# Kernel tuning notes

Hardware: AMD Instinct MI355X
Metric: run time of the kernel (lower is better)

## Reference

```python
import jax, jax.numpy as jnp
import numpy as np

H = 512   # hidden_size
V = 5000  # output_size (vocab)
B = 128   # batch
S = 64    # encoder source length
T = 52    # max_trajectory_length


def setup_inputs() -> dict:
    key = jax.random.key(0)
    ks = jax.random.split(key, 16)
    sc = 0.05
    rn = lambda k, shape: jax.random.normal(k, shape, dtype=jnp.float32) * sc
    return dict(
        encoder_outputs=jax.random.normal(ks[0], (B, S, H), dtype=jnp.float32),
        h0=jax.random.normal(ks[1], (1, B, H), dtype=jnp.float32),
        c0=jax.random.normal(ks[2], (1, B, H), dtype=jnp.float32),
        target_tensor=jax.random.randint(ks[3], (B, T), 0, V),
        emb=rn(ks[4], (V, H)),
        Wa=rn(ks[5], (H, H)), ba=jnp.zeros((H,), jnp.float32),
        Ua=rn(ks[6], (H, H)), bu=jnp.zeros((H,), jnp.float32),
        Va=rn(ks[7], (H,)), bv=jnp.zeros((), jnp.float32),
        W_ih=rn(ks[8], (4 * H, 2 * H)), W_hh=rn(ks[9], (4 * H, H)),
        b_ih=jnp.zeros((4 * H,), jnp.float32), b_hh=jnp.zeros((4 * H,), jnp.float32),
        Wout=rn(ks[10], (V, H)), bout=jnp.zeros((V,), jnp.float32),
    )


def reference(encoder_outputs, h0, c0, target_tensor, emb,
              Wa, ba, Ua, bu, Va, bv,
              W_ih, W_hh, b_ih, b_hh, Wout, bout):
    # Dropout is identity in eval mode.
    b = target_tensor.shape[0]
    # Ua(keys) is constant across decode steps -> precompute once. [B,S,H]
    keys_proj = jnp.einsum('bsh,kh->bsk', encoder_outputs, Ua) + bu
    # Teacher forcing: input at step i is target[:, i-1], step 0 is token 0.
    tokens = jnp.concatenate(
        [jnp.zeros((b, 1), target_tensor.dtype), target_tensor[:, :-1]], axis=1)  # [B,T]

    def step(carry, tok):
        h, c = carry                                # [B,H] each
        x = emb[tok]                                # embedding lookup [B,H]
        q = h @ Wa.T + ba                           # Wa(query) [B,H]
        scores = jnp.tanh(q[:, None, :] + keys_proj) @ Va + bv  # [B,S]
        w = jax.nn.softmax(scores, axis=-1)         # attn weights [B,S]
        ctx = jnp.einsum('bs,bsh->bh', w, encoder_outputs)       # context [B,H]
        xi = jnp.concatenate([x, ctx], axis=-1)     # [B,2H]
        gates = xi @ W_ih.T + b_ih + h @ W_hh.T + b_hh           # [B,4H]
        i_g, f_g, g_g, o_g = jnp.split(gates, 4, axis=-1)        # torch gate order i,f,g,o
        c = jax.nn.sigmoid(f_g) * c + jax.nn.sigmoid(i_g) * jnp.tanh(g_g)
        h = jax.nn.sigmoid(o_g) * jnp.tanh(c)
        logits = h @ Wout.T + bout                  # [B,V]
        return (h, c), (logits, w)

    (h, c), (logits, attn) = jax.lax.scan(step, (h0[0], c0[0]), tokens.T)
    logits = jnp.transpose(logits, (1, 0, 2))       # [B,T,V]
    log_probs = jax.nn.log_softmax(logits, axis=-1)
    attn = jnp.transpose(attn, (1, 0, 2))           # [B,T,S]
    return log_probs, (h[None], c[None]), attn
```

## Files before the change

kernel.cpp:

```cpp
#include <hip/hip_runtime.h>
#include <math.h>

#define H 512
#define V 5000
#define BB 128
#define SS 64
#define TT 52
#define NB 160

typedef __attribute__((ext_vector_type(8))) short bf16x8;
typedef __attribute__((ext_vector_type(4))) float f32x4;
typedef __attribute__((ext_vector_type(2))) float f32x2;

__device__ __forceinline__ unsigned short f2b(float f) {
    unsigned u = __float_as_uint(f);
    return (unsigned short)((u + 0x7fffu + ((u >> 16) & 1u)) >> 16);
}
__device__ __forceinline__ float b2f(unsigned short u) {
    return __uint_as_float((unsigned)u << 16);
}
__device__ __forceinline__ float ftanh(float x) {
    return 1.f - 2.f / (1.f + __expf(2.f * x));
}
__device__ __forceinline__ float fsig(float x) {
    return 1.f / (1.f + __expf(-x));
}
__device__ __forceinline__ unsigned char f2fp8(float f) {
    return (unsigned char)__builtin_amdgcn_cvt_pk_fp8_f32(f, f, 0, 0);
}

__device__ __forceinline__ void cld_row16(const unsigned short* p, bf16x8* r)
{
    asm volatile(
        "global_load_dwordx4 %0, %16, off sc0 sc1\n\t"
        "global_load_dwordx4 %1, %16, off offset:64 sc0 sc1\n\t"
        "global_load_dwordx4 %2, %16, off offset:128 sc0 sc1\n\t"
        "global_load_dwordx4 %3, %16, off offset:192 sc0 sc1\n\t"
        "global_load_dwordx4 %4, %16, off offset:256 sc0 sc1\n\t"
        "global_load_dwordx4 %5, %16, off offset:320 sc0 sc1\n\t"
        "global_load_dwordx4 %6, %16, off offset:384 sc0 sc1\n\t"
        "global_load_dwordx4 %7, %16, off offset:448 sc0 sc1\n\t"
        "global_load_dwordx4 %8, %16, off offset:512 sc0 sc1\n\t"
        "global_load_dwordx4 %9, %16, off offset:576 sc0 sc1\n\t"
        "global_load_dwordx4 %10, %16, off offset:640 sc0 sc1\n\t"
        "global_load_dwordx4 %11, %16, off offset:704 sc0 sc1\n\t"
        "global_load_dwordx4 %12, %16, off offset:768 sc0 sc1\n\t"
        "global_load_dwordx4 %13, %16, off offset:832 sc0 sc1\n\t"
        "global_load_dwordx4 %14, %16, off offset:896 sc0 sc1\n\t"
        "global_load_dwordx4 %15, %16, off offset:960 sc0 sc1\n\t"
        "s_waitcnt vmcnt(0)"
        : "=v"(r[0]), "=v"(r[1]), "=v"(r[2]), "=v"(r[3]),
          "=v"(r[4]), "=v"(r[5]), "=v"(r[6]), "=v"(r[7]),
          "=v"(r[8]), "=v"(r[9]), "=v"(r[10]), "=v"(r[11]),
          "=v"(r[12]), "=v"(r[13]), "=v"(r[14]), "=v"(r[15])
        : "v"(p) : "memory");
}
__device__ __forceinline__ void cld_f_2(const float* p0, const float* p1,
                                        float& a, float& b)
{
    asm volatile(
        "global_load_dword %0, %2, off sc0 sc1\n\t"
        "global_load_dword %1, %3, off sc0 sc1\n\t"
        "s_waitcnt vmcnt(0)"
        : "=v"(a), "=v"(b) : "v"(p0), "v"(p1) : "memory");
}
__device__ __forceinline__ void cld_f4p(const float* p, f32x4& a, f32x4& b)
{
    asm volatile(
        "global_load_dwordx4 %0, %2, off sc0 sc1\n\t"
        "global_load_dwordx4 %1, %2, off offset:16 sc0 sc1\n\t"
        "s_waitcnt vmcnt(0)"
        : "=v"(a), "=v"(b) : "v"(p) : "memory");
}
__device__ __forceinline__ void cst_f(float* p, float v)
{
    asm volatile("global_store_dword %0, %1, off sc0 sc1"
                 :: "v"(p), "v"(v) : "memory");
}
__device__ __forceinline__ void cst_u32(unsigned* p, unsigned v)
{
    asm volatile("global_store_dword %0, %1, off sc0 sc1"
                 :: "v"(p), "v"(v) : "memory");
}
__device__ __forceinline__ void cst_h(unsigned short* p, unsigned short v)
{
    unsigned vv = v;
    asm volatile("global_store_short %0, %1, off sc0 sc1"
                 :: "v"(p), "v"(vv) : "memory");
}

__global__ __launch_bounds__(256)
void prep_w(const float* __restrict__ Wa, const float* __restrict__ Whh,
            const float* __restrict__ Wih,
            const float* __restrict__ ba, const float* __restrict__ bih,
            const float* __restrict__ bhh,
            const float* __restrict__ Ua, const float* __restrict__ Wout,
            const float* __restrict__ enc,
            unsigned short* __restrict__ Wbig, unsigned short* __restrict__ Wc,
            unsigned short* __restrict__ Uab, unsigned short* __restrict__ Woutb,
            unsigned short* __restrict__ encb, float* __restrict__ bbig)
{
    const int stride = gridDim.x * blockDim.x;
    const int t0 = blockIdx.x * blockDim.x + threadIdx.x;
    for (int idx = t0; idx < 2560 * 1024; idx += stride) {
        const int j = idx >> 10, k = idx & 1023;
        float v;
        if (j < H) v = (k < H) ? Wa[j * H + k] : 0.f;
        else { const int n = j - H; v = (k < H) ? Whh[n * H + k] : Wih[n * 2 * H + (k - H)]; }
        Wbig[idx] = f2b(v);
    }
    for (int idx = t0; idx < 2048 * 512; idx += stride) {
        const int n = idx >> 9, k = idx & 511;
        Wc[idx] = f2b(Wih[n * 2 * H + H + k]);
    }
    for (int idx = t0; idx < 512 * 512; idx += stride)   Uab[idx]   = f2b(Ua[idx]);
    for (int idx = t0; idx < V * 512; idx += stride)     Woutb[idx] = f2b(Wout[idx]);
    for (int idx = t0; idx < BB * SS * H; idx += stride) encb[idx]  = f2b(enc[idx]);
    for (int j = t0; j < 2560; j += stride)
        bbig[j] = (j < H) ? ba[j] : bih[j - H] + bhh[j - H];
}

__global__ __launch_bounds__(256)
void gather_x(const float* __restrict__ emb, const int* __restrict__ tgt,
              unsigned short* __restrict__ xall)
{
    const int stride = gridDim.x * blockDim.x;
    for (int idx = blockIdx.x * blockDim.x + threadIdx.x; idx < TT * BB * H; idx += stride) {
        const int k = idx & 511;
        const int row = idx >> 9;
        const int t = row >> 7, b = row & 127;
        const int tok = (t == 0) ? 0 : tgt[b * TT + t - 1];
        xall[idx] = f2b(emb[(size_t)tok * H + k]);
    }
}

template<int OUT_MODE, int PERMUTE>
__global__ __launch_bounds__(256, 2)
void gemm_mfma(const unsigned short* __restrict__ A,
               const unsigned short* __restrict__ B,
               const float* __restrict__ bias,
               float* __restrict__ Cf, unsigned short* __restrict__ Cb,
               unsigned char* __restrict__ C8,
               int M, int N)
{
    __shared__ unsigned short As[128][72];
    __shared__ unsigned short Bs[128][72];
    const int tid = threadIdx.x;
    const int m0 = blockIdx.y * 128, n0 = blockIdx.x * 128;
    const int lane = tid & 63, wv = tid >> 6;
    const int qm = (wv >> 1) * 64, qn = (wv & 1) * 64;
    const int fr = lane & 15, fg = lane >> 4;
    f32x4 acc[4][4];
#pragma unroll
    for (int i = 0; i < 4; ++i)
#pragma unroll
        for (int j = 0; j < 4; ++j) acc[i][j] = (f32x4){0.f, 0.f, 0.f, 0.f};

    const int srow = tid >> 3, sc = (tid & 7) * 8;
    for (int k0 = 0; k0 < H; k0 += 64) {
#pragma unroll
        for (int u = 0; u < 4; ++u) {
            const int row = srow + u * 32;
            *(uint4*)&As[row][sc] = *(const uint4*)&A[(size_t)(m0 + row) * H + k0 + sc];
            int nr = n0 + row; if (nr > N - 1) nr = N - 1;
            *(uint4*)&Bs[row][sc] = *(const uint4*)&B[(size_t)nr * H + k0 + sc];
        }
        __syncthreads();
#pragma unroll
        for (int ks = 0; ks < 2; ++ks) {
            const int kk = ks * 32 + fg * 8;
            bf16x8 av[4], bv[4];
#pragma unroll
            for (int i = 0; i < 4; ++i) {
                av[i] = *(const bf16x8*)&As[qm + i * 16 + fr][kk];
                bv[i] = *(const bf16x8*)&Bs[qn + i * 16 + fr][kk];
            }
#pragma unroll
            for (int i = 0; i < 4; ++i)
#pragma unroll
                for (int j = 0; j < 4; ++j)
                    acc[i][j] = __builtin_amdgcn_mfma_f32_16x16x32_bf16(av[i], bv[j], acc[i][j], 0, 0, 0);
        }
        __syncthreads();
    }
#pragma unroll
    for (int i = 0; i < 4; ++i) {
        const int r0 = m0 + qm + i * 16 + fg * 4;
#pragma unroll
        for (int j = 0; j < 4; ++j) {
            const int col = n0 + qn + j * 16 + fr;
            if (col < N) {
                const float bi = bias ? bias[col] : 0.f;
#pragma unroll
                for (int v = 0; v < 4; ++v) {
                    const int r = r0 + v;
                    const float val = acc[i][j][v] + bi;
                    if (OUT_MODE == 1) {
                        Cb[(size_t)r * N + col] = f2b(val);
                    } else if (OUT_MODE == 2) {
                        C8[(size_t)r * N + col] = f2fp8(val);
                    } else {
                        const size_t orow = PERMUTE ? ((size_t)(r & (BB - 1)) * TT + (r >> 7))
                                                    : (size_t)r;
                        Cf[orow * (size_t)N + col] = val;
                    }
                }
            }
        }
    }
}

__device__ __forceinline__ void signal_flag(unsigned* flags, unsigned step)
{
    __syncthreads();
    if (threadIdx.x == 0)
        __hip_atomic_store(&flags[blockIdx.x * 32], step, __ATOMIC_RELAXED,
                           __HIP_MEMORY_SCOPE_AGENT);
}
__device__ __forceinline__ void wait_flags(unsigned* flags, int lo, int hi,
                                           unsigned step)
{
    for (int i = lo + (int)threadIdx.x; i < hi; i += 256) {
        while (__hip_atomic_load(&flags[i * 32], __ATOMIC_RELAXED,
                                 __HIP_MEMORY_SCOPE_AGENT) < step)
            __builtin_amdgcn_s_sleep(1);
    }
    __syncthreads();
}

struct PParams {
    const float* h0;
    const float* c0;
    const unsigned short* keysb;
    const unsigned char* encW8;
    const float* Va;
    const float* bv;
    const float* bbig;
    const unsigned short* Wbig;
    const unsigned short* xall;
    unsigned short* hbf;
    float* Y;
    unsigned short* hallb;
    float* attn;
    float* out_h;
    float* out_c;
    unsigned* flags;
};

__global__ __launch_bounds__(256, 1)
void persist(PParams p)
{
    __shared__ unsigned short WA[16][1032];
    __shared__ float qa_s[H];
    __shared__ float va_s[H];
    __shared__ float part[SS][4];
    __shared__ float wbuf[SS];
    __shared__ float gbuf[4 * H];
    __shared__ float cs[H];

    const int tid  = threadIdx.x;
    const int beta = blockIdx.x;
    unsigned bs = 1;

    for (int i = beta * 256 + tid; i < BB * H; i += NB * 256)
        cst_h(&p.hbf[i], f2b(p.h0[i]));
    {
        const int j0 = beta * 16;
        for (int idx = tid; idx < 16 * 128; idx += 256) {
            const int r = idx >> 7, ch = idx & 127;
            *(uint4*)&WA[r][ch * 8] = *(const uint4*)&p.Wbig[(size_t)(j0 + r) * 1024 + ch * 8];
        }
    }
    if (beta < 128) {
        for (int j = tid; j < H; j += 256) cs[j] = p.c0[beta * H + j];
        for (int i = tid; i < H; i += 256) va_s[i] = p.Va[i];
    }
    signal_flag(p.flags, bs);
    wait_flags(p.flags, 0, NB, bs);
    ++bs;

    for (int t = 0; t < TT; ++t) {
        {
            const int j0 = beta * 16;
            const int wv = tid >> 6, lane = tid & 63;
            const int r = lane & 15, g = lane >> 4;
            const int b0 = wv * 32, b1 = b0 + 16;
            const int ko = g * 8;
            bf16x8 hr0[16], hr1[16];
            cld_row16(p.hbf + (size_t)(b0 + r) * H + ko, hr0);
            cld_row16(p.hbf + (size_t)(b1 + r) * H + ko, hr1);
            f32x4 acc0 = {0.f, 0.f, 0.f, 0.f};
            f32x4 acc1 = {0.f, 0.f, 0.f, 0.f};
#pragma unroll
            for (int ks = 0; ks < 16; ++ks) {
                bf16x8 bf = *(const bf16x8*)&WA[r][ks * 32 + ko];
                acc0 = __builtin_amdgcn_mfma_f32_16x16x32_bf16(hr0[ks], bf, acc0, 0, 0, 0);
                acc1 = __builtin_amdgcn_mfma_f32_16x16x32_bf16(hr1[ks], bf, acc1, 0, 0, 0);
            }
            const unsigned short* x0p = p.xall + ((size_t)t * BB + b0 + r) * H + ko;
            const unsigned short* x1p = p.xall + ((size_t)t * BB + b1 + r) * H + ko;
#pragma unroll
            for (int ks = 0; ks < 16; ++ks) {
                bf16x8 bf = *(const bf16x8*)&WA[r][512 + ks * 32 + ko];
                acc0 = __builtin_amdgcn_mfma_f32_16x16x32_bf16(*(const bf16x8*)&x0p[ks * 32], bf, acc0, 0, 0, 0);
                acc1 = __builtin_amdgcn_mfma_f32_16x16x32_bf16(*(const bf16x8*)&x1p[ks * 32], bf, acc1, 0, 0, 0);
            }
            const float bb = p.bbig[j0 + r];
#pragma unroll
            for (int i = 0; i < 4; ++i) {
                cst_f(p.Y + (size_t)(b0 + g * 4 + i) * 2560 + j0 + r, acc0[i] + bb);
                cst_f(p.Y + (size_t)(b1 + g * 4 + i) * 2560 + j0 + r, acc1[i] + bb);
            }
        }
        signal_flag(p.flags, bs);

        if (beta < 128) {
            const int b = beta;
            const float* yrow = p.Y + (size_t)b * 2560;
            wait_flags(p.flags, 0, 32, bs);
            cld_f_2(yrow + tid, yrow + 256 + tid, qa_s[tid], qa_s[tid + 256]);
            __syncthreads();
            const int s = tid >> 2, q = tid & 3;
            const unsigned short* kp = p.keysb + ((size_t)b * SS + s) * H + q * 128;
            const float* qp = qa_s + q * 128;
            const float* vp = va_s + q * 128;
            float a2 = 0.f, a2b = 0.f;
#pragma unroll 4
            for (int i = 0; i < 128; i += 2) {
                a2  += ftanh(qp[i] + b2f(kp[i])) * vp[i];
                a2b += ftanh(qp[i + 1] + b2f(kp[i + 1])) * vp[i + 1];
            }
            part[s][q] = a2 + a2b;
            __syncthreads();
            if (tid < 64) {
                float sc = part[tid][0] + part[tid][1] + part[tid][2] + part[tid][3] + p.bv[0];
                float m = sc;
                for (int o = 32; o; o >>= 1) m = fmaxf(m, __shfl_xor(m, o));
                const float e = __expf(sc - m);
                float ss = e;
                for (int o = 32; o; o >>= 1) ss += __shfl_xor(ss, o);
                const float w = e / ss;
                wbuf[tid] = w;
                p.attn[((size_t)b * TT + t) * SS + tid] = w;
            }
            wait_flags(p.flags, 32, NB, bs);
            {
                float gc[8] = {0.f, 0.f, 0.f, 0.f, 0.f, 0.f, 0.f, 0.f};
                const unsigned char* ew = p.encW8 + (size_t)b * SS * 2048 + tid * 8;
#pragma unroll 8
                for (int s2 = 0; s2 < SS; ++s2) {
                    const float w2 = wbuf[s2];
                    const uint2 u = *(const uint2*)(ew + (size_t)s2 * 2048);
                    const f32x2 e01 = __builtin_amdgcn_cvt_pk_f32_fp8(u.x, 0);
                    const f32x2 e23 = __builtin_amdgcn_cvt_pk_f32_fp8(u.x, 1);
                    const f32x2 e45 = __builtin_amdgcn_cvt_pk_f32_fp8(u.y, 0);
                    const f32x2 e67 = __builtin_amdgcn_cvt_pk_f32_fp8(u.y, 1);
                    gc[0] += w2 * e01[0]; gc[1] += w2 * e01[1];
                    gc[2] += w2 * e23[0]; gc[3] += w2 * e23[1];
                    gc[4] += w2 * e45[0]; gc[5] += w2 * e45[1];
                    gc[6] += w2 * e67[0]; gc[7] += w2 * e67[1];
                }
                f32x4 y0, y1;
                cld_f4p(yrow + 512 + tid * 8, y0, y1);
#pragma unroll
                for (int i = 0; i < 4; ++i) {
                    gbuf[tid * 8 + i]     = gc[i] + y0[i];
                    gbuf[tid * 8 + 4 + i] = gc[4 + i] + y1[i];
                }
            }
            __syncthreads();
            {
                const int last = (t == TT - 1);
                unsigned hpack = 0;
                float hn2[2], cn2[2];
#pragma unroll
                for (int u = 0; u < 2; ++u) {
                    const int j = tid * 2 + u;
                    const float ig = gbuf[j];
                    const float fg = gbuf[512 + j];
                    const float gg = gbuf[1024 + j];
                    const float og = gbuf[1536 + j];
                    const float co = cs[j];
                    const float cn = fsig(fg) * co + fsig(ig) * ftanh(gg);
                    const float hn = fsig(og) * ftanh(cn);
                    cs[j] = cn;
                    hn2[u] = hn; cn2[u] = cn;
                    hpack |= ((unsigned)f2b(hn)) << (16 * u);
                }
                cst_u32((unsigned*)&p.hbf[b * H + tid * 2], hpack);
                *(unsigned*)&p.hallb[((size_t)t * BB + b) * H + tid * 2] = hpack;
                if (last) {
#pragma unroll
                    for (int u = 0; u < 2; ++u) {
                        p.out_h[b * H + tid * 2 + u] = hn2[u];
                        p.out_c[b * H + tid * 2 + u] = cn2[u];
                    }
                }
            }
        }
        signal_flag(p.flags, bs + 1);
        wait_flags(p.flags, 0, NB, bs + 1);
        bs += 2;
    }
}

__global__ __launch_bounds__(256)
void logsoftmax_rows(float* __restrict__ P)
{
    __shared__ float red[256];
    float* p = P + (size_t)blockIdx.x * V;
    const int tid = threadIdx.x;
    float m = -1e30f;
    for (int i = tid; i < V; i += 256) m = fmaxf(m, p[i]);
    red[tid] = m; __syncthreads();
    for (int sft = 128; sft; sft >>= 1) {
        if (tid < sft) red[tid] = fmaxf(red[tid], red[tid + sft]);
        __syncthreads();
    }
    m = red[0]; __syncthreads();
    float ssum = 0.f;
    for (int i = tid; i < V; i += 256) ssum += __expf(p[i] - m);
    red[tid] = ssum; __syncthreads();
    for (int sft = 128; sft; sft >>= 1) {
        if (tid < sft) red[tid] += red[tid + sft];
        __syncthreads();
    }
    const float lse = m + __logf(red[0]);
    for (int i = tid; i < V; i += 256) p[i] -= lse;
}

extern "C" void kernel_launch(void* const* d_in, const int* in_sizes, int n_in,
                              void* d_out, int out_size, void* d_ws, size_t ws_size,
                              hipStream_t stream)
{
    (void)in_sizes; (void)n_in; (void)out_size; (void)ws_size;
    const float* enc  = (const float*)d_in[0];
    const float* h0   = (const float*)d_in[1];
    const float* c0   = (const float*)d_in[2];
    const int*   tgt  = (const int*)  d_in[3];
    const float* emb  = (const float*)d_in[4];
    const float* Wa   = (const float*)d_in[5];
    const float* ba   = (const float*)d_in[6];
    const float* Ua   = (const float*)d_in[7];
    const float* bu   = (const float*)d_in[8];
    const float* Va   = (const float*)d_in[9];
    const float* bv   = (const float*)d_in[10];
    const float* Wih  = (const float*)d_in[11];
    const float* Whh  = (const float*)d_in[12];
    const float* bih  = (const float*)d_in[13];
    const float* bhh  = (const float*)d_in[14];
    const float* Wout = (const float*)d_in[15];
    const float* bout = (const float*)d_in[16];

    float* ws = (float*)d_ws;
    float* Y    = ws;
    float* bbig = Y + 327680;
    unsigned* flags = (unsigned*)(bbig + 2560);
    unsigned short* Wbig  = (unsigned short*)(flags + 5504);
    unsigned short* Wc    = Wbig + 2621440;
    unsigned short* Uab   = Wc + 1048576;
    unsigned short* Woutb = Uab + 262144;
    unsigned short* encb  = Woutb + 2560000;
    unsigned short* keysb = encb + 4194304;
    unsigned short* xall  = keysb + 4194304;
    unsigned short* hallb = xall + 3407872;
    unsigned short* hbf   = hallb + 3407872;
    unsigned char*  encW8 = (unsigned char*)(hbf + 65536);

    float* out    = (float*)d_out;
    float* out_h  = out + (size_t)BB * TT * V;
    float* out_c  = out_h + BB * H;
    float* out_at = out_c + BB * H;

    hipMemsetAsync(flags, 0, 5504 * sizeof(unsigned), stream);

    prep_w<<<dim3(2048), dim3(256), 0, stream>>>(
        Wa, Whh, Wih, ba, bih, bhh, Ua, Wout, enc, Wbig, Wc, Uab, Woutb, encb, bbig);
    gather_x<<<dim3(512), dim3(256), 0, stream>>>(emb, tgt, xall);

    gemm_mfma<1, 0><<<dim3(4, 64), dim3(256), 0, stream>>>(
        encb, Uab, bu, nullptr, keysb, nullptr, BB * SS, H);
    gemm_mfma<2, 0><<<dim3(16, 64), dim3(256), 0, stream>>>(
        encb, Wc, nullptr, nullptr, nullptr, encW8, BB * SS, 2048);

    PParams pp;
    pp.h0 = h0; pp.c0 = c0; pp.keysb = keysb; pp.encW8 = encW8;
    pp.Va = Va; pp.bv = bv; pp.bbig = bbig;
    pp.Wbig = Wbig; pp.xall = xall;
    pp.hbf = hbf; pp.Y = Y; pp.hallb = hallb;
    pp.attn = out_at; pp.out_h = out_h; pp.out_c = out_c;
    pp.flags = flags;
    persist<<<dim3(NB), dim3(256), 0, stream>>>(pp);

    gemm_mfma<0, 1><<<dim3(40, 52), dim3(256), 0, stream>>>(
        hallb, Woutb, bout, out, nullptr, nullptr, TT * BB, V);
    logsoftmax_rows<<<dim3(BB * TT), dim3(256), 0, stream>>>(out);
}
```

Baseline: 1.465 ms.

## Replace per-step global barrier with fine-grained per-row flag waits

Drops the end-of-step all-block barrier. Each wave now waits only on the flags of the 32 batch rows whose hidden state it reads before loading them. Block-to-column assignment is remapped so the last 32 blocks compute the query projection, and the attention blocks wait only on those before starting. The two row loads are issued back-to-back with a single wait, and the flag protocol gains a separate per-step hidden-ready signal. This trades the global barrier's latency for more complex dependency tracking, with the risk of ordering or visibility bugs.

```diff
diff --git a/kernel.cpp b/kernel.cpp
--- a/kernel.cpp
+++ b/kernel.cpp
@@ -29,31 +29,37 @@
     return (unsigned char)__builtin_amdgcn_cvt_pk_fp8_f32(f, f, 0, 0);
 }
 
+#define CLD16_BODY \
+        "global_load_dwordx4 %0, %16, off sc0 sc1\n\t"              \
+        "global_load_dwordx4 %1, %16, off offset:64 sc0 sc1\n\t"    \
+        "global_load_dwordx4 %2, %16, off offset:128 sc0 sc1\n\t"   \
+        "global_load_dwordx4 %3, %16, off offset:192 sc0 sc1\n\t"   \
+        "global_load_dwordx4 %4, %16, off offset:256 sc0 sc1\n\t"   \
+        "global_load_dwordx4 %5, %16, off offset:320 sc0 sc1\n\t"   \
+        "global_load_dwordx4 %6, %16, off offset:384 sc0 sc1\n\t"   \
+        "global_load_dwordx4 %7, %16, off offset:448 sc0 sc1\n\t"   \
+        "global_load_dwordx4 %8, %16, off offset:512 sc0 sc1\n\t"   \
+        "global_load_dwordx4 %9, %16, off offset:576 sc0 sc1\n\t"   \
+        "global_load_dwordx4 %10, %16, off offset:640 sc0 sc1\n\t"  \
+        "global_load_dwordx4 %11, %16, off offset:704 sc0 sc1\n\t"  \
+        "global_load_dwordx4 %12, %16, off offset:768 sc0 sc1\n\t"  \
+        "global_load_dwordx4 %13, %16, off offset:832 sc0 sc1\n\t"  \
+        "global_load_dwordx4 %14, %16, off offset:896 sc0 sc1\n\t"  \
+        "global_load_dwordx4 %15, %16, off offset:960 sc0 sc1"
+#define CLD16_OUTS(r) \
+          "=v"(r[0]), "=v"(r[1]), "=v"(r[2]), "=v"(r[3]),   \
+          "=v"(r[4]), "=v"(r[5]), "=v"(r[6]), "=v"(r[7]),   \
+          "=v"(r[8]), "=v"(r[9]), "=v"(r[10]), "=v"(r[11]), \
+          "=v"(r[12]), "=v"(r[13]), "=v"(r[14]), "=v"(r[15])
+
+__device__ __forceinline__ void cld_row16_nw(const unsigned short* p, bf16x8* r)
+{
+    asm volatile(CLD16_BODY : CLD16_OUTS(r) : "v"(p) : "memory");
+}
 __device__ __forceinline__ void cld_row16(const unsigned short* p, bf16x8* r)
 {
-    asm volatile(
-        "global_load_dwordx4 %0, %16, off sc0 sc1\n\t"
-        "global_load_dwordx4 %1, %16, off offset:64 sc0 sc1\n\t"
-        "global_load_dwordx4 %2, %16, off offset:128 sc0 sc1\n\t"
-        "global_load_dwordx4 %3, %16, off offset:192 sc0 sc1\n\t"
-        "global_load_dwordx4 %4, %16, off offset:256 sc0 sc1\n\t"
-        "global_load_dwordx4 %5, %16, off offset:320 sc0 sc1\n\t"
-        "global_load_dwordx4 %6, %16, off offset:384 sc0 sc1\n\t"
-        "global_load_dwordx4 %7, %16, off offset:448 sc0 sc1\n\t"
-        "global_load_dwordx4 %8, %16, off offset:512 sc0 sc1\n\t"
-        "global_load_dwordx4 %9, %16, off offset:576 sc0 sc1\n\t"
-        "global_load_dwordx4 %10, %16, off offset:640 sc0 sc1\n\t"
-        "global_load_dwordx4 %11, %16, off offset:704 sc0 sc1\n\t"
-        "global_load_dwordx4 %12, %16, off offset:768 sc0 sc1\n\t"
-        "global_load_dwordx4 %13, %16, off offset:832 sc0 sc1\n\t"
-        "global_load_dwordx4 %14, %16, off offset:896 sc0 sc1\n\t"
-        "global_load_dwordx4 %15, %16, off offset:960 sc0 sc1\n\t"
-        "s_waitcnt vmcnt(0)"
-        : "=v"(r[0]), "=v"(r[1]), "=v"(r[2]), "=v"(r[3]),
-          "=v"(r[4]), "=v"(r[5]), "=v"(r[6]), "=v"(r[7]),
-          "=v"(r[8]), "=v"(r[9]), "=v"(r[10]), "=v"(r[11]),
-          "=v"(r[12]), "=v"(r[13]), "=v"(r[14]), "=v"(r[15])
-        : "v"(p) : "memory");
+    asm volatile(CLD16_BODY "\n\ts_waitcnt vmcnt(0)"
+                 : CLD16_OUTS(r) : "v"(p) : "memory");
 }
 __device__ __forceinline__ void cld_f_2(const float* p0, const float* p1,
                                         float& a, float& b)
@@ -226,6 +232,16 @@
             __builtin_amdgcn_s_sleep(1);
     }
     __syncthreads();
+}
+__device__ __forceinline__ void wait_flags_wave32(unsigned* flags, int lo,
+                                                  unsigned step)
+{
+    const int lane = threadIdx.x & 63;
+    if (lane < 32) {
+        while (__hip_atomic_load(&flags[(lo + lane) * 32], __ATOMIC_RELAXED,
+                                 __HIP_MEMORY_SCOPE_AGENT) < step)
+            __builtin_amdgcn_s_sleep(1);
+    }
 }
 
 struct PParams {
@@ -260,35 +276,34 @@
 
     const int tid  = threadIdx.x;
     const int beta = blockIdx.x;
-    unsigned bs = 1;
+    const int j0   = (beta < 128) ? (512 + beta * 16) : ((beta - 128) * 16);
 
     for (int i = beta * 256 + tid; i < BB * H; i += NB * 256)
         cst_h(&p.hbf[i], f2b(p.h0[i]));
-    {
-        const int j0 = beta * 16;
-        for (int idx = tid; idx < 16 * 128; idx += 256) {
-            const int r = idx >> 7, ch = idx & 127;
-            *(uint4*)&WA[r][ch * 8] = *(const uint4*)&p.Wbig[(size_t)(j0 + r) * 1024 + ch * 8];
-        }
+    for (int idx = tid; idx < 16 * 128; idx += 256) {
+        const int r = idx >> 7, ch = idx & 127;
+        *(uint4*)&WA[r][ch * 8] = *(const uint4*)&p.Wbig[(size_t)(j0 + r) * 1024 + ch * 8];
     }
     if (beta < 128) {
         for (int j = tid; j < H; j += 256) cs[j] = p.c0[beta * H + j];
         for (int i = tid; i < H; i += 256) va_s[i] = p.Va[i];
     }
-    signal_flag(p.flags, bs);
-    wait_flags(p.flags, 0, NB, bs);
-    ++bs;
+    signal_flag(p.flags, 1);
+    wait_flags(p.flags, 0, NB, 1);
 
     for (int t = 0; t < TT; ++t) {
+        const unsigned sp1 = 2 * t + 2;
+        const unsigned sh  = 2 * t + 3;
         {
-            const int j0 = beta * 16;
             const int wv = tid >> 6, lane = tid & 63;
             const int r = lane & 15, g = lane >> 4;
             const int b0 = wv * 32, b1 = b0 + 16;
             const int ko = g * 8;
+            wait_flags_wave32(p.flags, b0, sp1 - 1);
             bf16x8 hr0[16], hr1[16];
-            cld_row16(p.hbf + (size_t)(b0 + r) * H + ko, hr0);
-            cld_row16(p.hbf + (size_t)(b1 + r) * H + ko, hr1);
+            cld_row16_nw(p.hbf + (size_t)(b0 + r) * H + ko, hr0);
+            cld_row16  (p.hbf + (size_t)(b1 + r) * H + ko, hr1);
+            __builtin_amdgcn_sched_barrier(0);
             f32x4 acc0 = {0.f, 0.f, 0.f, 0.f};
             f32x4 acc1 = {0.f, 0.f, 0.f, 0.f};
 #pragma unroll
@@ -312,12 +327,12 @@
                 cst_f(p.Y + (size_t)(b1 + g * 4 + i) * 2560 + j0 + r, acc1[i] + bb);
             }
         }
-        signal_flag(p.flags, bs);
+        signal_flag(p.flags, sp1);
 
         if (beta < 128) {
             const int b = beta;
             const float* yrow = p.Y + (size_t)b * 2560;
-            wait_flags(p.flags, 0, 32, bs);
+            wait_flags(p.flags, 128, NB, sp1);
             cld_f_2(yrow + tid, yrow + 256 + tid, qa_s[tid], qa_s[tid + 256]);
             __syncthreads();
             const int s = tid >> 2, q = tid & 3;
@@ -343,7 +358,7 @@
                 wbuf[tid] = w;
                 p.attn[((size_t)b * TT + t) * SS + tid] = w;
             }
-            wait_flags(p.flags, 32, NB, bs);
+            wait_flags(p.flags, 0, 128, sp1);
             {
                 float gc[8] = {0.f, 0.f, 0.f, 0.f, 0.f, 0.f, 0.f, 0.f};
                 const unsigned char* ew = p.encW8 + (size_t)b * SS * 2048 + tid * 8;
@@ -397,10 +412,8 @@
                     }
                 }
             }
+            signal_flag(p.flags, sh);
         }
-        signal_flag(p.flags, bs + 1);
-        wait_flags(p.flags, 0, NB, bs + 1);
-        bs += 2;
     }
 }
 
```

Measured after the change: 1.444 ms. About the same (-1.4%).

## Split persistent LSTM into independent batch groups with local flags; precompute input gates

Applied to the files above, without the earlier changes.

Replaces the global all-block barrier of the persistent decode kernel with 8 independent groups of 16 blocks, each handling 16 batch rows and syncing only through per-group h and Y flags. The embedding contribution to the gates is moved into a separate up-front GEMM (xgates), so the recurrent step only multiplies h by the Wa and Whh rows. Each block now computes 160 gate rows, 96 held in LDS and the rest streamed from global memory. This cuts grid-wide synchronisation latency per step, at the cost of an extra large precompute GEMM, a bigger workspace, and redundant weight reads across groups.

```diff
diff --git a/kernel.cpp b/kernel.cpp
--- a/kernel.cpp
+++ b/kernel.cpp
@@ -6,7 +6,9 @@
 #define BB 128
 #define SS 64
 #define TT 52
-#define NB 160
+#define GSZ 16
+#define NBLK 128
+#define LROWS 96
 
 typedef __attribute__((ext_vector_type(8))) short bf16x8;
 typedef __attribute__((ext_vector_type(4))) float f32x4;
@@ -29,34 +31,38 @@
     return (unsigned char)__builtin_amdgcn_cvt_pk_fp8_f32(f, f, 0, 0);
 }
 
-__device__ __forceinline__ void cld_row16(const unsigned short* p, bf16x8* r)
+__device__ __forceinline__ void pollf(unsigned* a, unsigned s)
+{
+    for (;;) {
+        unsigned v;
+        asm volatile("global_load_dword %0, %1, off sc0 sc1\n\ts_waitcnt vmcnt(0)"
+                     : "=v"(v) : "v"(a) : "memory");
+        if (v >= s) break;
+        __builtin_amdgcn_s_sleep(1);
+    }
+}
+__device__ __forceinline__ void fst(unsigned* p, unsigned v)
+{
+    asm volatile("global_store_dword %0, %1, off sc0 sc1" :: "v"(p), "v"(v) : "memory");
+}
+__device__ __forceinline__ void cstf4(float* p, f32x4 v)
+{
+    asm volatile("global_store_dwordx4 %0, %1, off sc0 sc1" :: "v"(p), "v"(v) : "memory");
+}
+__device__ __forceinline__ void cld4x16B(const unsigned short* p0, const unsigned short* p1,
+                                         const unsigned short* p2, const unsigned short* p3,
+                                         uint4& a, uint4& b, uint4& c, uint4& d)
 {
     asm volatile(
-        "global_load_dwordx4 %0, %16, off sc0 sc1\n\t"
-        "global_load_dwordx4 %1, %16, off offset:64 sc0 sc1\n\t"
-        "global_load_dwordx4 %2, %16, off offset:128 sc0 sc1\n\t"
-        "global_load_dwordx4 %3, %16, off offset:192 sc0 sc1\n\t"
-        "global_load_dwordx4 %4, %16, off offset:256 sc0 sc1\n\t"
-        "global_load_dwordx4 %5, %16, off offset:320 sc0 sc1\n\t"
-        "global_load_dwordx4 %6, %16, off offset:384 sc0 sc1\n\t"
-        "global_load_dwordx4 %7, %16, off offset:448 sc0 sc1\n\t"
-        "global_load_dwordx4 %8, %16, off offset:512 sc0 sc1\n\t"
-        "global_load_dwordx4 %9, %16, off offset:576 sc0 sc1\n\t"
-        "global_load_dwordx4 %10, %16, off offset:640 sc0 sc1\n\t"
-        "global_load_dwordx4 %11, %16, off offset:704 sc0 sc1\n\t"
-        "global_load_dwordx4 %12, %16, off offset:768 sc0 sc1\n\t"
-        "global_load_dwordx4 %13, %16, off offset:832 sc0 sc1\n\t"
-        "global_load_dwordx4 %14, %16, off offset:896 sc0 sc1\n\t"
-        "global_load_dwordx4 %15, %16, off offset:960 sc0 sc1\n\t"
+        "global_load_dwordx4 %0, %4, off sc0 sc1\n\t"
+        "global_load_dwordx4 %1, %5, off sc0 sc1\n\t"
+        "global_load_dwordx4 %2, %6, off sc0 sc1\n\t"
+        "global_load_dwordx4 %3, %7, off sc0 sc1\n\t"
         "s_waitcnt vmcnt(0)"
-        : "=v"(r[0]), "=v"(r[1]), "=v"(r[2]), "=v"(r[3]),
-          "=v"(r[4]), "=v"(r[5]), "=v"(r[6]), "=v"(r[7]),
-          "=v"(r[8]), "=v"(r[9]), "=v"(r[10]), "=v"(r[11]),
-          "=v"(r[12]), "=v"(r[13]), "=v"(r[14]), "=v"(r[15])
-        : "v"(p) : "memory");
-}
-__device__ __forceinline__ void cld_f_2(const float* p0, const float* p1,
-                                        float& a, float& b)
+        : "=v"(a), "=v"(b), "=v"(c), "=v"(d)
+        : "v"(p0), "v"(p1), "v"(p2), "v"(p3) : "memory");
+}
+__device__ __forceinline__ void cldf2(const float* p0, const float* p1, float& a, float& b)
 {
     asm volatile(
         "global_load_dword %0, %2, off sc0 sc1\n\t"
@@ -64,29 +70,25 @@
         "s_waitcnt vmcnt(0)"
         : "=v"(a), "=v"(b) : "v"(p0), "v"(p1) : "memory");
 }
-__device__ __forceinline__ void cld_f4p(const float* p, f32x4& a, f32x4& b)
+__device__ __forceinline__ void cldf8s(const float* p, float* r)
 {
     asm volatile(
-        "global_load_dwordx4 %0, %2, off sc0 sc1\n\t"
-        "global_load_dwordx4 %1, %2, off offset:16 sc0 sc1\n\t"
+        "global_load_dword %0, %8, off sc0 sc1\n\t"
+        "global_load_dword %1, %8, off offset:64 sc0 sc1\n\t"
+        "global_load_dword %2, %8, off offset:128 sc0 sc1\n\t"
+        "global_load_dword %3, %8, off offset:192 sc0 sc1\n\t"
+        "global_load_dword %4, %8, off offset:256 sc0 sc1\n\t"
+        "global_load_dword %5, %8, off offset:320 sc0 sc1\n\t"
+        "global_load_dword %6, %8, off offset:384 sc0 sc1\n\t"
+        "global_load_dword %7, %8, off offset:448 sc0 sc1\n\t"
         "s_waitcnt vmcnt(0)"
-        : "=v"(a), "=v"(b) : "v"(p) : "memory");
-}
-__device__ __forceinline__ void cst_f(float* p, float v)
-{
-    asm volatile("global_store_dword %0, %1, off sc0 sc1"
-                 :: "v"(p), "v"(v) : "memory");
-}
-__device__ __forceinline__ void cst_u32(unsigned* p, unsigned v)
-{
-    asm volatile("global_store_dword %0, %1, off sc0 sc1"
-                 :: "v"(p), "v"(v) : "memory");
-}
-__device__ __forceinline__ void cst_h(unsigned short* p, unsigned short v)
-{
-    unsigned vv = v;
-    asm volatile("global_store_short %0, %1, off sc0 sc1"
-                 :: "v"(p), "v"(vv) : "memory");
+        : "=v"(r[0]), "=v"(r[1]), "=v"(r[2]), "=v"(r[3]),
+          "=v"(r[4]), "=v"(r[5]), "=v"(r[6]), "=v"(r[7])
+        : "v"(p) : "memory");
+}
+__device__ __forceinline__ void cstu32c(unsigned* p, unsigned v)
+{
+    asm volatile("global_store_dword %0, %1, off sc0 sc1" :: "v"(p), "v"(v) : "memory");
 }
 
 __global__ __launch_bounds__(256)
@@ -96,22 +98,21 @@
             const float* __restrict__ bhh,
             const float* __restrict__ Ua, const float* __restrict__ Wout,
             const float* __restrict__ enc,
-            unsigned short* __restrict__ Wbig, unsigned short* __restrict__ Wc,
+            unsigned short* __restrict__ Whb, unsigned short* __restrict__ Wxb,
+            unsigned short* __restrict__ Wc,
             unsigned short* __restrict__ Uab, unsigned short* __restrict__ Woutb,
             unsigned short* __restrict__ encb, float* __restrict__ bbig)
 {
     const int stride = gridDim.x * blockDim.x;
     const int t0 = blockIdx.x * blockDim.x + threadIdx.x;
-    for (int idx = t0; idx < 2560 * 1024; idx += stride) {
-        const int j = idx >> 10, k = idx & 1023;
-        float v;
-        if (j < H) v = (k < H) ? Wa[j * H + k] : 0.f;
-        else { const int n = j - H; v = (k < H) ? Whh[n * H + k] : Wih[n * 2 * H + (k - H)]; }
-        Wbig[idx] = f2b(v);
+    for (int idx = t0; idx < 2560 * 512; idx += stride) {
+        const int j = idx >> 9, k = idx & 511;
+        Whb[idx] = f2b((j < H) ? Wa[j * H + k] : Whh[(j - H) * H + k]);
     }
     for (int idx = t0; idx < 2048 * 512; idx += stride) {
         const int n = idx >> 9, k = idx & 511;
-        Wc[idx] = f2b(Wih[n * 2 * H + H + k]);
+        Wxb[idx] = f2b(Wih[n * 2 * H + k]);
+        Wc[idx]  = f2b(Wih[n * 2 * H + H + k]);
     }
     for (int idx = t0; idx < 512 * 512; idx += stride)   Uab[idx]   = f2b(Ua[idx]);
     for (int idx = t0; idx < V * 512; idx += stride)     Woutb[idx] = f2b(Wout[idx]);
@@ -195,11 +196,9 @@
                 for (int v = 0; v < 4; ++v) {
                     const int r = r0 + v;
                     const float val = acc[i][j][v] + bi;
-                    if (OUT_MODE == 1) {
-                        Cb[(size_t)r * N + col] = f2b(val);
-                    } else if (OUT_MODE == 2) {
-                        C8[(size_t)r * N + col] = f2fp8(val);
-                    } else {
+                    if (OUT_MODE == 1) Cb[(size_t)r * N + col] = f2b(val);
+                    else if (OUT_MODE == 2) C8[(size_t)r * N + col] = f2fp8(val);
+                    else {
                         const size_t orow = PERMUTE ? ((size_t)(r & (BB - 1)) * TT + (r >> 7))
                                                     : (size_t)r;
                         Cf[orow * (size_t)N + col] = val;
@@ -208,24 +207,6 @@
             }
         }
     }
-}
-
-__device__ __forceinline__ void signal_flag(unsigned* flags, unsigned step)
-{
-    __syncthreads();
-    if (threadIdx.x == 0)
-        __hip_atomic_store(&flags[blockIdx.x * 32], step, __ATOMIC_RELAXED,
-                           __HIP_MEMORY_SCOPE_AGENT);
-}
-__device__ __forceinline__ void wait_flags(unsigned* flags, int lo, int hi,
-                                           unsigned step)
-{
-    for (int i = lo + (int)threadIdx.x; i < hi; i += 256) {
-        while (__hip_atomic_load(&flags[i * 32], __ATOMIC_RELAXED,
-                                 __HIP_MEMORY_SCOPE_AGENT) < step)
-            __builtin_amdgcn_s_sleep(1);
-    }
-    __syncthreads();
 }
 
 struct PParams {
@@ -236,21 +217,23 @@
     const float* Va;
     const float* bv;
     const float* bbig;
-    const unsigned short* Wbig;
-    const unsigned short* xall;
-    unsigned short* hbf;
-    float* Y;
+    const unsigned short* Whb;
+    const unsigned short* xgates;
+    unsigned short* hbuf;
+    float* Ybuf;
     unsigned short* hallb;
     float* attn;
     float* out_h;
     float* out_c;
-    unsigned* flags;
+    unsigned* hfl;
+    unsigned* yfl;
 };
 
 __global__ __launch_bounds__(256, 1)
 void persist(PParams p)
 {
-    __shared__ unsigned short WA[16][1032];
+    __shared__ unsigned short WA[LROWS][520];
+    __shared__ unsigned short h_s[16][520];
     __shared__ float qa_s[H];
     __shared__ float va_s[H];
     __shared__ float part[SS][4];
@@ -260,147 +243,173 @@
 
     const int tid  = threadIdx.x;
     const int beta = blockIdx.x;
-    unsigned bs = 1;
-
-    for (int i = beta * 256 + tid; i < BB * H; i += NB * 256)
-        cst_h(&p.hbf[i], f2b(p.h0[i]));
+    const int grp  = beta & 7;
+    const int slot = beta >> 3;
+    const int gb   = grp * GSZ + slot;
+    const int gi   = gb;
+    const int wv   = tid >> 6, lane = tid & 63;
+    const int fr   = lane & 15, fg = lane >> 4;
+
+    unsigned short* hbg = p.hbuf + (size_t)grp * GSZ * H;
+    float* ybg = p.Ybuf + (size_t)grp * 2560 * GSZ;
+
+    for (int idx = tid; idx < LROWS * 64; idx += 256) {
+        const int r = idx >> 6, c = idx & 63;
+        *(uint4*)&WA[r][c * 8] =
+            *(const uint4*)&p.Whb[((size_t)slot * 160 + r) * H + c * 8];
+    }
+    for (int j = tid; j < H; j += 256) {
+        cs[j] = p.c0[(size_t)gb * H + j];
+        va_s[j] = p.Va[j];
+    }
     {
-        const int j0 = beta * 16;
-        for (int idx = tid; idx < 16 * 128; idx += 256) {
-            const int r = idx >> 7, ch = idx & 127;
-            *(uint4*)&WA[r][ch * 8] = *(const uint4*)&p.Wbig[(size_t)(j0 + r) * 1024 + ch * 8];
-        }
-    }
-    if (beta < 128) {
-        for (int j = tid; j < H; j += 256) cs[j] = p.c0[beta * H + j];
-        for (int i = tid; i < H; i += 256) va_s[i] = p.Va[i];
-    }
-    signal_flag(p.flags, bs);
-    wait_flags(p.flags, 0, NB, bs);
-    ++bs;
+        const float* hp = p.h0 + (size_t)gb * H;
+        const unsigned hp32 = (unsigned)f2b(hp[tid * 2]) |
+                              ((unsigned)f2b(hp[tid * 2 + 1]) << 16);
+        cstu32c((unsigned*)(hbg + (size_t)slot * H) + tid, hp32);
+    }
+    __syncthreads();
+    if (tid == 0) fst(&p.hfl[gi * 32], 1u);
 
     for (int t = 0; t < TT; ++t) {
+        const unsigned st = (unsigned)(t + 1);
+        if (tid < GSZ) pollf(&p.hfl[(grp * GSZ + tid) * 32], st);
+        __syncthreads();
         {
-            const int j0 = beta * 16;
-            const int wv = tid >> 6, lane = tid & 63;
-            const int r = lane & 15, g = lane >> 4;
-            const int b0 = wv * 32, b1 = b0 + 16;
-            const int ko = g * 8;
-            bf16x8 hr0[16], hr1[16];
-            cld_row16(p.hbf + (size_t)(b0 + r) * H + ko, hr0);
-            cld_row16(p.hbf + (size_t)(b1 + r) * H + ko, hr1);
-            f32x4 acc0 = {0.f, 0.f, 0.f, 0.f};
-            f32x4 acc1 = {0.f, 0.f, 0.f, 0.f};
-#pragma unroll
-            for (int ks = 0; ks < 16; ++ks) {
-                bf16x8 bf = *(const bf16x8*)&WA[r][ks * 32 + ko];
-                acc0 = __builtin_amdgcn_mfma_f32_16x16x32_bf16(hr0[ks], bf, acc0, 0, 0, 0);
-                acc1 = __builtin_amdgcn_mfma_f32_16x16x32_bf16(hr1[ks], bf, acc1, 0, 0, 0);
-            }
-            const unsigned short* x0p = p.xall + ((size_t)t * BB + b0 + r) * H + ko;
-            const unsigned short* x1p = p.xall + ((size_t)t * BB + b1 + r) * H + ko;
-#pragma unroll
-            for (int ks = 0; ks < 16; ++ks) {
-                bf16x8 bf = *(const bf16x8*)&WA[r][512 + ks * 32 + ko];
-                acc0 = __builtin_amdgcn_mfma_f32_16x16x32_bf16(*(const bf16x8*)&x0p[ks * 32], bf, acc0, 0, 0, 0);
-                acc1 = __builtin_amdgcn_mfma_f32_16x16x32_bf16(*(const bf16x8*)&x1p[ks * 32], bf, acc1, 0, 0, 0);
-            }
-            const float bb = p.bbig[j0 + r];
-#pragma unroll
-            for (int i = 0; i < 4; ++i) {
-                cst_f(p.Y + (size_t)(b0 + g * 4 + i) * 2560 + j0 + r, acc0[i] + bb);
-                cst_f(p.Y + (size_t)(b1 + g * 4 + i) * 2560 + j0 + r, acc1[i] + bb);
-            }
-        }
-        signal_flag(p.flags, bs);
-
-        if (beta < 128) {
-            const int b = beta;
-            const float* yrow = p.Y + (size_t)b * 2560;
-            wait_flags(p.flags, 0, 32, bs);
-            cld_f_2(yrow + tid, yrow + 256 + tid, qa_s[tid], qa_s[tid + 256]);
-            __syncthreads();
+            uint4 a, b, c4, d;
+            cld4x16B(hbg + (size_t)tid * 8, hbg + (size_t)(tid + 256) * 8,
+                     hbg + (size_t)(tid + 512) * 8, hbg + (size_t)(tid + 768) * 8,
+                     a, b, c4, d);
+            const int r0 = tid >> 6, c0 = (tid & 63) * 8;
+            *(uint4*)&h_s[r0][c0]      = a;
+            *(uint4*)&h_s[r0 + 4][c0]  = b;
+            *(uint4*)&h_s[r0 + 8][c0]  = c4;
+            *(uint4*)&h_s[r0 + 12][c0] = d;
+        }
+        __syncthreads();
+        for (int tt = wv; tt < 10; tt += 4) {
+            const int jrow = slot * 160 + tt * 16 + fr;
+            f32x4 acc = {0.f, 0.f, 0.f, 0.f};
+            if (tt < 6) {
+#pragma unroll
+                for (int ks = 0; ks < 16; ++ks) {
+                    bf16x8 A = *(const bf16x8*)&h_s[fr][ks * 32 + fg * 8];
+                    bf16x8 B = *(const bf16x8*)&WA[tt * 16 + fr][ks * 32 + fg * 8];
+                    acc = __builtin_amdgcn_mfma_f32_16x16x32_bf16(A, B, acc, 0, 0, 0);
+                }
+            } else {
+                const unsigned short* wr = p.Whb + (size_t)jrow * H;
+#pragma unroll
+                for (int ks = 0; ks < 16; ++ks) {
+                    bf16x8 A = *(const bf16x8*)&h_s[fr][ks * 32 + fg * 8];
+                    bf16x8 B = *(const bf16x8*)&wr[ks * 32 + fg * 8];
+                    acc = __builtin_amdgcn_mfma_f32_16x16x32_bf16(A, B, acc, 0, 0, 0);
+                }
+            }
+            const float bb = p.bbig[jrow];
+            f32x4 o;
+#pragma unroll
+            for (int i = 0; i < 4; ++i) o[i] = acc[i] + bb;
+            cstf4(ybg + (size_t)jrow * GSZ + fg * 4, o);
+        }
+        __syncthreads();
+        if (tid == 0) fst(&p.yfl[gi * 32], st);
+
+        if (tid < 4) pollf(&p.yfl[(grp * GSZ + tid) * 32], st);
+        __syncthreads();
+        cldf2(ybg + (size_t)tid * GSZ + slot,
+              ybg + (size_t)(tid + 256) * GSZ + slot,
+              qa_s[tid], qa_s[tid + 256]);
+        __syncthreads();
+        {
             const int s = tid >> 2, q = tid & 3;
-            const unsigned short* kp = p.keysb + ((size_t)b * SS + s) * H + q * 128;
+            const unsigned short* kp = p.keysb + ((size_t)gb * SS + s) * H + q * 128;
             const float* qp = qa_s + q * 128;
             const float* vp = va_s + q * 128;
             float a2 = 0.f, a2b = 0.f;
-#pragma unroll 4
-            for (int i = 0; i < 128; i += 2) {
-                a2  += ftanh(qp[i] + b2f(kp[i])) * vp[i];
-                a2b += ftanh(qp[i + 1] + b2f(kp[i + 1])) * vp[i + 1];
+#pragma unroll
+            for (int i8 = 0; i8 < 16; ++i8) {
+                bf16x8 kv = *(const bf16x8*)&kp[i8 * 8];
+#pragma unroll
+                for (int u = 0; u < 8; u += 2) {
+                    const int i = i8 * 8 + u;
+                    a2  += ftanh(qp[i]     + b2f((unsigned short)kv[u]))     * vp[i];
+                    a2b += ftanh(qp[i + 1] + b2f((unsigned short)kv[u + 1])) * vp[i + 1];
+                }
             }
             part[s][q] = a2 + a2b;
-            __syncthreads();
-            if (tid < 64) {
-                float sc = part[tid][0] + part[tid][1] + part[tid][2] + part[tid][3] + p.bv[0];
-                float m = sc;
-                for (int o = 32; o; o >>= 1) m = fmaxf(m, __shfl_xor(m, o));
-                const float e = __expf(sc - m);
-                float ss = e;
-                for (int o = 32; o; o >>= 1) ss += __shfl_xor(ss, o);
-                const float w = e / ss;
-                wbuf[tid] = w;
-                p.attn[((size_t)b * TT + t) * SS + tid] = w;
-            }
-            wait_flags(p.flags, 32, NB, bs);
-            {
-                float gc[8] = {0.f, 0.f, 0.f, 0.f, 0.f, 0.f, 0.f, 0.f};
-                const unsigned char* ew = p.encW8 + (size_t)b * SS * 2048 + tid * 8;
+        }
+        __syncthreads();
+        if (tid < 64) {
+            float sc = part[tid][0] + part[tid][1] + part[tid][2] + part[tid][3] + p.bv[0];
+            float m = sc;
+            for (int o = 32; o; o >>= 1) m = fmaxf(m, __shfl_xor(m, o));
+            const float e = __expf(sc - m);
+            float ss = e;
+            for (int o = 32; o; o >>= 1) ss += __shfl_xor(ss, o);
+            const float w = e / ss;
+            wbuf[tid] = w;
+            p.attn[((size_t)gb * TT + t) * SS + tid] = w;
+        }
+        __syncthreads();
+        float gc[8] = {0.f, 0.f, 0.f, 0.f, 0.f, 0.f, 0.f, 0.f};
+        {
+            const unsigned char* ew = p.encW8 + (size_t)gb * SS * 2048 + tid * 8;
 #pragma unroll 8
-                for (int s2 = 0; s2 < SS; ++s2) {
-                    const float w2 = wbuf[s2];
-                    const uint2 u = *(const uint2*)(ew + (size_t)s2 * 2048);
-                    const f32x2 e01 = __builtin_amdgcn_cvt_pk_f32_fp8(u.x, 0);
-                    const f32x2 e23 = __builtin_amdgcn_cvt_pk_f32_fp8(u.x, 1);
-                    const f32x2 e45 = __builtin_amdgcn_cvt_pk_f32_fp8(u.y, 0);
-                    const f32x2 e67 = __builtin_amdgcn_cvt_pk_f32_fp8(u.y, 1);
-                    gc[0] += w2 * e01[0]; gc[1] += w2 * e01[1];
-                    gc[2] += w2 * e23[0]; gc[3] += w2 * e23[1];
-                    gc[4] += w2 * e45[0]; gc[5] += w2 * e45[1];
-                    gc[6] += w2 * e67[0]; gc[7] += w2 * e67[1];
+            for (int s2 = 0; s2 < SS; ++s2) {
+                const float w2 = wbuf[s2];
+                const uint2 u = *(const uint2*)(ew + (size_t)s2 * 2048);
+                const f32x2 e01 = __builtin_amdgcn_cvt_pk_f32_fp8(u.x, 0);
+                const f32x2 e23 = __builtin_amdgcn_cvt_pk_f32_fp8(u.x, 1);
+                const f32x2 e45 = __builtin_amdgcn_cvt_pk_f32_fp8(u.y, 0);
+                const f32x2 e67 = __builtin_amdgcn_cvt_pk_f32_fp8(u.y, 1);
+                gc[0] += w2 * e01[0]; gc[1] += w2 * e01[1];
+                gc[2] += w2 * e23[0]; gc[3] += w2 * e23[1];
+                gc[4] += w2 * e45[0]; gc[5] += w2 * e45[1];
+                gc[6] += w2 * e67[0]; gc[7] += w2 * e67[1];
+            }
+        }
+        if (tid < GSZ) pollf(&p.yfl[(grp * GSZ + tid) * 32], st);
+        __syncthreads();
+        {
+            float yg[8];
+            cldf8s(ybg + (size_t)(512 + tid * 8) * GSZ + slot, yg);
+            bf16x8 xg = *(const bf16x8*)&p.xgates[((size_t)t * BB + gb) * 2048 + tid * 8];
+#pragma unroll
+            for (int i = 0; i < 8; ++i)
+                gbuf[tid * 8 + i] = gc[i] + yg[i] + b2f((unsigned short)xg[i]);
+        }
+        __syncthreads();
+        {
+            const int last = (t == TT - 1);
+            unsigned hpack = 0;
+            float hn2[2], cn2[2];
+#pragma unroll
+            for (int u = 0; u < 2; ++u) {
+                const int j = tid * 2 + u;
+                const float ig  = gbuf[j];
+                const float fgt = gbuf[512 + j];
+                const float gg  = gbuf[1024 + j];
+                const float og  = gbuf[1536 + j];
+                const float co  = cs[j];
+                const float cn = fsig(fgt) * co + fsig(ig) * ftanh(gg);
+                const float hn = fsig(og) * ftanh(cn);
+                cs[j] = cn;
+                hn2[u] = hn; cn2[u] = cn;
+                hpack |= ((unsigned)f2b(hn)) << (16 * u);
+            }
+            cstu32c((unsigned*)(hbg + (size_t)slot * H) + tid, hpack);
+            *(unsigned*)&p.hallb[((size_t)t * BB + gb) * H + tid * 2] = hpack;
+            if (last) {
+#pragma unroll
+                for (int u = 0; u < 2; ++u) {
+                    p.out_h[gb * H + tid * 2 + u] = hn2[u];
+                    p.out_c[gb * H + tid * 2 + u] = cn2[u];
                 }
-                f32x4 y0, y1;
-                cld_f4p(yrow + 512 + tid * 8, y0, y1);
-#pragma unroll
-                for (int i = 0; i < 4; ++i) {
-                    gbuf[tid * 8 + i]     = gc[i] + y0[i];
-                    gbuf[tid * 8 + 4 + i] = gc[4 + i] + y1[i];
-                }
-            }
-            __syncthreads();
-            {
-                const int last = (t == TT - 1);
-                unsigned hpack = 0;
-                float hn2[2], cn2[2];
-#pragma unroll
-                for (int u = 0; u < 2; ++u) {
-                    const int j = tid * 2 + u;
-                    const float ig = gbuf[j];
-                    const float fg = gbuf[512 + j];
-                    const float gg = gbuf[1024 + j];
-                    const float og = gbuf[1536 + j];
-                    const float co = cs[j];
-                    const float cn = fsig(fg) * co + fsig(ig) * ftanh(gg);
-                    const float hn = fsig(og) * ftanh(cn);
-                    cs[j] = cn;
-                    hn2[u] = hn; cn2[u] = cn;
-                    hpack |= ((unsigned)f2b(hn)) << (16 * u);
-                }
-                cst_u32((unsigned*)&p.hbf[b * H + tid * 2], hpack);
-                *(unsigned*)&p.hallb[((size_t)t * BB + b) * H + tid * 2] = hpack;
-                if (last) {
-#pragma unroll
-                    for (int u = 0; u < 2; ++u) {
-                        p.out_h[b * H + tid * 2 + u] = hn2[u];
-                        p.out_c[b * H + tid * 2 + u] = cn2[u];
-                    }
-                }
-            }
-        }
-        signal_flag(p.flags, bs + 1);
-        wait_flags(p.flags, 0, NB, bs + 1);
-        bs += 2;
+            }
+        }
+        __syncthreads();
+        if (tid == 0) fst(&p.hfl[gi * 32], st + 1);
     }
 }
 
@@ -453,44 +462,51 @@
     const float* bout = (const float*)d_in[16];
 
     float* ws = (float*)d_ws;
-    float* Y    = ws;
-    float* bbig = Y + 327680;
-    unsigned* flags = (unsigned*)(bbig + 2560);
-    unsigned short* Wbig  = (unsigned short*)(flags + 5504);
-    unsigned short* Wc    = Wbig + 2621440;
+    float* bbig = ws;
+    float* Ybuf = bbig + 2560;
+    unsigned* flags = (unsigned*)(Ybuf + 327680);
+    unsigned* hfl = flags;
+    unsigned* yfl = flags + 4096;
+    unsigned short* Whb   = (unsigned short*)(flags + 8192);
+    unsigned short* Wxb   = Whb + 1310720;
+    unsigned short* Wc    = Wxb + 1048576;
     unsigned short* Uab   = Wc + 1048576;
     unsigned short* Woutb = Uab + 262144;
     unsigned short* encb  = Woutb + 2560000;
     unsigned short* keysb = encb + 4194304;
     unsigned short* xall  = keysb + 4194304;
-    unsigned short* hallb = xall + 3407872;
-    unsigned short* hbf   = hallb + 3407872;
-    unsigned char*  encW8 = (unsigned char*)(hbf + 65536);
+    unsigned short* xgates= xall + 3407872;
+    unsigned short* hallb = xgates + 13631488;
+    unsigned short* hbuf  = hallb + 3407872;
+    unsigned char*  encW8 = (unsigned char*)(hbuf + 65536);
 
     float* out    = (float*)d_out;
     float* out_h  = out + (size_t)BB * TT * V;
     float* out_c  = out_h + BB * H;
     float* out_at = out_c + BB * H;
 
-    hipMemsetAsync(flags, 0, 5504 * sizeof(unsigned), stream);
+    hipMemsetAsync(flags, 0, 8192 * sizeof(unsigned), stream);
 
     prep_w<<<dim3(2048), dim3(256), 0, stream>>>(
-        Wa, Whh, Wih, ba, bih, bhh, Ua, Wout, enc, Wbig, Wc, Uab, Woutb, encb, bbig);
+        Wa, Whh, Wih, ba, bih, bhh, Ua, Wout, enc,
+        Whb, Wxb, Wc, Uab, Woutb, encb, bbig);
     gather_x<<<dim3(512), dim3(256), 0, stream>>>(emb, tgt, xall);
 
     gemm_mfma<1, 0><<<dim3(4, 64), dim3(256), 0, stream>>>(
         encb, Uab, bu, nullptr, keysb, nullptr, BB * SS, H);
     gemm_mfma<2, 0><<<dim3(16, 64), dim3(256), 0, stream>>>(
         encb, Wc, nullptr, nullptr, nullptr, encW8, BB * SS, 2048);
+    gemm_mfma<1, 0><<<dim3(16, 52), dim3(256), 0, stream>>>(
+        xall, Wxb, nullptr, nullptr, xgates, nullptr, TT * BB, 2048);
 
     PParams pp;
     pp.h0 = h0; pp.c0 = c0; pp.keysb = keysb; pp.encW8 = encW8;
     pp.Va = Va; pp.bv = bv; pp.bbig = bbig;
-    pp.Wbig = Wbig; pp.xall = xall;
-    pp.hbf = hbf; pp.Y = Y; pp.hallb = hallb;
+    pp.Whb = Whb; pp.xgates = xgates;
+    pp.hbuf = hbuf; pp.Ybuf = Ybuf; pp.hallb = hallb;
     pp.attn = out_at; pp.out_h = out_h; pp.out_c = out_c;
-    pp.flags = flags;
-    persist<<<dim3(NB), dim3(256), 0, stream>>>(pp);
+    pp.hfl = hfl; pp.yfl = yfl;
+    persist<<<dim3(NBLK), dim3(256), 0, stream>>>(pp);
 
     gemm_mfma<0, 1><<<dim3(40, 52), dim3(256), 0, stream>>>(
         hallb, Woutb, bout, out, nullptr, nullptr, TT * BB, V);
```

Measured after the change: 1.273 ms. 13.1% less time.
